# Performance work log

Measured on AMD Instinct MI355X. Metric: run time of the kernel, lower is better.

Reference implementation:

```python
import jax, jax.numpy as jnp
import numpy as np

T, B, D, H, O = 128, 256, 512, 1024, 20
THR = 1.0
ALPHA = float(np.exp(-1.0 / 20.0))  # exp(-dt/tau_m)
KAPPA = float(np.exp(-1.0 / 20.0))  # exp(-dt/tau_o)
B_O = 0.0


def setup_inputs() -> dict:
    key = jax.random.key(0)
    k1, k2, k3, k4 = jax.random.split(key, 4)
    x = jax.random.normal(k1, (T, B, D), dtype=jnp.float32)
    # kaiming_normal: std = sqrt(2/fan_in), gain = 1.0
    w_in = jax.random.normal(k2, (H, D), dtype=jnp.float32) * np.sqrt(2.0 / D)
    w_rec = jax.random.normal(k3, (H, H), dtype=jnp.float32) * np.sqrt(2.0 / H)
    w_out = jax.random.normal(k4, (O, H), dtype=jnp.float32) * np.sqrt(2.0 / H)
    return {"x": x, "w_in": w_in, "w_rec": w_rec, "w_out": w_out}


def reference(x, w_in, w_rec, w_out):
    # mask out self-recurrence (diagonal zeroed)
    w_rec_eff = w_rec * (1.0 - jnp.eye(w_rec.shape[0], dtype=w_rec.dtype))

    def step(carry, x_t):
        v, z, vo = carry
        v_new = ALPHA * v + z @ w_rec_eff.T + x_t @ w_in.T - z * THR
        z_new = (v_new > THR).astype(v_new.dtype)
        vo_new = KAPPA * vo + z_new @ w_out.T + B_O
        return (v_new, z_new, vo_new), vo_new

    v0 = jnp.zeros((x.shape[1], w_rec.shape[0]), dtype=x.dtype)
    vo0 = jnp.zeros((x.shape[1], w_out.shape[0]), dtype=x.dtype)
    # torch loop runs t = 0..T-2, consuming x[0..T-2]; vo[0] stays zero
    _, vo_rest = jax.lax.scan(step, (v0, v0, vo0), x[:-1])
    vo = jnp.concatenate([vo0[None], vo_rest], axis=0)  # [T, B, O]
    return jax.nn.softmax(vo, axis=2)
```

## Files before the change

kernel.cpp:

```cpp
#include <hip/hip_runtime.h>
#include <math.h>


#define T_ 128
#define B_ 256
#define D_ 512
#define H_ 1024
#define O_ 20
#define ST_ 127
#define WPB 32
#define ALPHA_F ((float)0.95122942450071400909)
#define KAPPA_F ((float)0.95122942450071400909)

typedef float v2f __attribute__((ext_vector_type(2)));

#if defined(__has_builtin)
#if __has_builtin(__builtin_elementwise_fma)
#define PK_FMA(a, b, c) __builtin_elementwise_fma(a, b, c)
#endif
#if __has_builtin(__builtin_amdgcn_global_load_lds)
#define HAVE_GLL 1
#endif
#endif
#ifndef PK_FMA
static __device__ inline v2f pk_fma_impl(v2f a, v2f b, v2f c) {
    v2f r; r[0] = __fmaf_rn(a[0], b[0], c[0]); r[1] = __fmaf_rn(a[1], b[1], c[1]);
    return r;
}
#define PK_FMA(a, b, c) pk_fma_impl(a, b, c)
#endif

static __device__ __forceinline__ void f2acc(float2& a, const float2 b) {
    a.x = __fadd_rn(a.x, b.x);
    a.y = __fadd_rn(a.y, b.y);
}

static __device__ __forceinline__ unsigned spread16(unsigned x) {
    x &= 0xFFFFu;
    x = (x | (x << 8)) & 0x00FF00FFu;
    x = (x | (x << 4)) & 0x0F0F0F0Fu;
    x = (x | (x << 2)) & 0x33333333u;
    x = (x | (x << 1)) & 0x55555555u;
    return x;
}

__global__ __launch_bounds__(256) void transpose_k(
    const float* __restrict__ src, float* __restrict__ dst,
    int rows, int cols, int zero_diag)
{
    __shared__ float tile[32][33];
    const int c0 = blockIdx.x * 32;
    const int r0 = blockIdx.y * 32;
    const int tid = threadIdx.x;
    const int lr = tid >> 3;
    const int lc = (tid & 7) * 4;
    const float4 vv = *(const float4*)(src + (size_t)(r0 + lr) * cols + c0 + lc);
    tile[lr][lc+0] = vv.x; tile[lr][lc+1] = vv.y;
    tile[lr][lc+2] = vv.z; tile[lr][lc+3] = vv.w;
    __syncthreads();
    const int wc = lr;
    const int wr = lc;
    float4 o;
    o.x = tile[wr+0][wc]; o.y = tile[wr+1][wc];
    o.z = tile[wr+2][wc]; o.w = tile[wr+3][wc];
    if (zero_diag) {
        const int c = c0 + wc;
        if (c == r0 + wr + 0) o.x = 0.f;
        if (c == r0 + wr + 1) o.y = 0.f;
        if (c == r0 + wr + 2) o.z = 0.f;
        if (c == r0 + wr + 3) o.w = 0.f;
    }
    *(float4*)(dst + (size_t)(c0 + wc) * rows + r0 + wr) = o;
}

__global__ __launch_bounds__(256) void srnn_init(
    float* __restrict__ v, unsigned* __restrict__ z0)
{
    const int i = blockIdx.x * 256 + threadIdx.x;
    if (i < B_ * H_)  v[i]  = 0.0f;
    if (i < B_ * WPB) z0[i] = 0u;
}

#define SWC(r) ((((r) >> 3) & 3) << 2)
__global__ __launch_bounds__(256) void srnn_qsum(
    const float* __restrict__ x,
    const float* __restrict__ WinT,
    float* __restrict__ qs,
    int s0, int nsl)
{
    __shared__ float wt[32][68];
    __shared__ float xt[32][68];
    const int nwg = nsl * 64;
    const int rb  = (int)blockIdx.x;
    const int lb  = (rb & 7) * (nwg >> 3) + (rb >> 3);
    const int sl = lb >> 6;
    const int t = lb & 63;
    const int h0 = (t & 15) << 6;
    const int b0 = (t >> 4) << 6;
    const int tid = threadIdx.x;
    const int tx4 = (tid & 15) << 2;
    const int ty4 = (tid >> 4) << 2;
    const float* xs = x + (size_t)(s0 + sl) * (B_ * D_);

    const int idxa = tid * 2, idxb = tid * 2 + 1;
    const int wra = idxa >> 4, wca = (idxa & 15) << 2;
    const int wrb = idxb >> 4, wcb = (idxb & 15) << 2;
    const int bra = idxa >> 3, kqa = (idxa & 7) << 2;
    const int brb = idxb >> 3, kqb = (idxb & 7) << 2;

    v2f accA[4][2], accB[4][2];
    #pragma unroll
    for (int i = 0; i < 4; ++i) {
        accA[i][0]=(v2f)0.f; accA[i][1]=(v2f)0.f;
        accB[i][0]=(v2f)0.f; accB[i][1]=(v2f)0.f;
    }

    float4 wp0, wp1, xp0, xp1;
    auto qload = [&](int kc) {
        wp0 = *(const float4*)(WinT + (size_t)(kc*32 + wra)*H_ + h0 + wca);
        wp1 = *(const float4*)(WinT + (size_t)(kc*32 + wrb)*H_ + h0 + wcb);
        xp0 = *(const float4*)(xs + (size_t)(b0+bra)*D_ + kc*32 + kqa);
        xp1 = *(const float4*)(xs + (size_t)(b0+brb)*D_ + kc*32 + kqb);
    };
    auto qstore = [&]() {
        *(float4*)&wt[wra][wca] = wp0;
        *(float4*)&wt[wrb][wcb] = wp1;
        xt[kqa+0][bra ^ SWC(kqa+0)]=xp0.x; xt[kqa+1][bra ^ SWC(kqa+1)]=xp0.y;
        xt[kqa+2][bra ^ SWC(kqa+2)]=xp0.z; xt[kqa+3][bra ^ SWC(kqa+3)]=xp0.w;
        xt[kqb+0][brb ^ SWC(kqb+0)]=xp1.x; xt[kqb+1][brb ^ SWC(kqb+1)]=xp1.y;
        xt[kqb+2][brb ^ SWC(kqb+2)]=xp1.z; xt[kqb+3][brb ^ SWC(kqb+3)]=xp1.w;
    };
    auto qinner = [&](v2f (&ACC)[4][2]) {
        #pragma unroll
        for (int kk = 0; kk < 32; ++kk) {
            const float4 zf = *(const float4*)&xt[kk][ty4 ^ SWC(kk)];
            const float4 wf = *(const float4*)&wt[kk][tx4];
            v2f wlo, whi;
            wlo[0]=wf.x; wlo[1]=wf.y; whi[0]=wf.z; whi[1]=wf.w;
            const float zz[4] = {zf.x, zf.y, zf.z, zf.w};
            #pragma unroll
            for (int i = 0; i < 4; ++i) {
                v2f zv; zv[0]=zz[i]; zv[1]=zz[i];
                ACC[i][0] = PK_FMA(zv, wlo, ACC[i][0]);
                ACC[i][1] = PK_FMA(zv, whi, ACC[i][1]);
            }
        }
    };

    qload(0);
    for (int kc = 0; kc < 10; ++kc) {
        __syncthreads();
        qstore();
        __syncthreads();
        qload(kc + 1);
        qinner(accA);
    }
    for (int kc = 10; kc < 16; ++kc) {
        __syncthreads();
        qstore();
        __syncthreads();
        if (kc < 15) qload(kc + 1);
        qinner(accB);
    }

    float* qd = qs + (size_t)sl * (B_ * H_);
    #pragma unroll
    for (int i = 0; i < 4; ++i) {
        float4 o;
        o.x = __fadd_rn(accA[i][0][0], accB[i][0][0]);
        o.y = __fadd_rn(accA[i][0][1], accB[i][0][1]);
        o.z = __fadd_rn(accA[i][1][0], accB[i][1][0]);
        o.w = __fadd_rn(accA[i][1][1], accB[i][1][1]);
        *(float4*)(qd + (size_t)(b0 + ty4 + i) * H_ + h0 + tx4) = o;
    }
}

#define STG_FLOATS (64 * 128)

static __device__ __forceinline__ void issue_stage(
    const float* __restrict__ WrecT, float (*wt)[STG_FLOATS],
    int s, int cb, int ht, int w, int ln)
{
#ifdef HAVE_GLL
    const int r2 = (ln >> 5);
    const int c4 = (ln & 31) << 2;
    #pragma unroll
    for (int i = 0; i < 4; ++i) {
        const int row = s * 64 + w * 8 + i * 2;
        const float* gs = WrecT + (size_t)(row + r2) * H_ + ht * 128 + c4;
        float* ld = &wt[cb][(w * 8 + i * 2) * 128];
        __builtin_amdgcn_global_load_lds(
            (const __attribute__((address_space(1))) void*)gs,
            (__attribute__((address_space(3))) void*)ld, 16, 0, 0);
    }
#else
    #pragma unroll
    for (int i = 0; i < 4; ++i) {
        const int row = s * 64 + w * 8 + i * 2 + (ln >> 5);
        const float4 tv = *(const float4*)(WrecT + (size_t)row * H_ + ht * 128 + ((ln & 31) << 2));
        *(float4*)&wt[cb][(w * 8 + i * 2) * 128 + ln * 4] = tv;
    }
#endif
}

#ifdef HAVE_GLL
#define WAITV4() asm volatile("s_waitcnt vmcnt(4)" ::: "memory")
#define WAITV0() asm volatile("s_waitcnt vmcnt(0)" ::: "memory")
#define STEPBAR() __builtin_amdgcn_s_barrier()
#else
#define WAITV4()
#define WAITV0()
#define STEPBAR() __syncthreads()
#endif

#define PROC_STAGE(ACC, SS, CB) do { \
    const int n_ = __builtin_amdgcn_readfirstlane(cntL[SS][w]); \
    const unsigned short* kl_ = klist2[SS][w]; \
    const char* wb_ = ((const char*)&wt[CB][0]) + (ln << 3); \
    int i_ = 0; \
    for (; i_ + 4 <= n_; i_ += 4) { \
        const uint2 kk_ = *(const uint2*)(kl_ + i_); \
        const float2 r0_ = *(const float2*)(wb_ + (kk_.x & 0xFFFFu)); \
        const float2 r1_ = *(const float2*)(wb_ + (kk_.x >> 16)); \
        const float2 r2_ = *(const float2*)(wb_ + (kk_.y & 0xFFFFu)); \
        const float2 r3_ = *(const float2*)(wb_ + (kk_.y >> 16)); \
        f2acc(ACC, r0_); f2acc(ACC, r1_); f2acc(ACC, r2_); f2acc(ACC, r3_); \
    } \
    if (i_ < n_) { \
        const uint2 kk_ = *(const uint2*)(kl_ + i_); \
        const float2 r0_ = *(const float2*)(wb_ + (kk_.x & 0xFFFFu)); \
        f2acc(ACC, r0_); \
        if (i_ + 1 < n_) { \
            const float2 r1_ = *(const float2*)(wb_ + (kk_.x >> 16)); \
            f2acc(ACC, r1_); \
        } \
        if (i_ + 2 < n_) { \
            const float2 r2_ = *(const float2*)(wb_ + (kk_.y & 0xFFFFu)); \
            f2acc(ACC, r2_); \
        } \
    } \
} while (0)

#define STEP_S(SS, ACC) do { \
    if ((SS) < 15) issue_stage(WrecT, wt, (SS) + 1, ((SS) + 1) & 1, ht, w, ln); \
    if ((SS) < 15) { WAITV4(); } else { WAITV0(); } \
    STEPBAR(); \
    asm volatile("" ::: "memory"); \
    PROC_STAGE(ACC, SS, (SS) & 1); \
    asm volatile("" ::: "memory"); \
    STEPBAR(); \
} while (0)

__global__ __launch_bounds__(512) void srnn_step(
    const float* __restrict__ WrecT,
    const float* __restrict__ qsum_s,
    const unsigned* __restrict__ zin,
    unsigned* __restrict__ zout,
    float* __restrict__ v)
{
    __shared__ float wt[2][STG_FLOATS];
    __shared__ unsigned short klist2[16][8][64];
    __shared__ int cntL[16][8];
    __shared__ unsigned zwsh[8][32];

    const int bid = (int)blockIdx.x;
    const int ht = bid & 7;
    const int bg = bid >> 3;
    const int tid = threadIdx.x;
    const int w = tid >> 6;
    const int ln = tid & 63;
    const int b = bg * 8 + w;

    unsigned zword = 0u;
    if (ln < 32) zword = zin[(size_t)b * WPB + ln];

    issue_stage(WrecT, wt, 0, 0, ht, w, ln);

    if (ln < 32) {
        zwsh[w][ln] = zword;
        const int myc = __popc(zword);
        const int ec = __shfl_up(myc, 1, 32);
        const int oc = __shfl_down(myc, 1, 32);
        if (!(ln & 1)) cntL[ln >> 1][w] = myc + oc;
        int ofs = (ln & 1) ? ec : 0;
        const unsigned kbase = (unsigned)((ln & 1) << 14);
        unsigned tw = zword;
        while (tw) {
            const int j = __builtin_ctz(tw);
            tw &= tw - 1;
            klist2[ln >> 1][w][ofs++] = (unsigned short)(kbase + ((unsigned)j << 9));
        }
    }

    float2 acc0 = {0.f, 0.f}, acc1 = {0.f, 0.f};
    float2 acc2 = {0.f, 0.f}, acc3 = {0.f, 0.f};

    STEP_S(0, acc0);  STEP_S(1, acc0);  STEP_S(2, acc0);  STEP_S(3, acc0);  STEP_S(4, acc0);
    STEP_S(5, acc1);  STEP_S(6, acc1);  STEP_S(7, acc1);  STEP_S(8, acc1);  STEP_S(9, acc1);
    STEP_S(10, acc2); STEP_S(11, acc2); STEP_S(12, acc2); STEP_S(13, acc2); STEP_S(14, acc2);
    STEP_S(15, acc3);

    const int h0 = ht * 128 + ln * 2;
    const size_t bh = (size_t)b * H_ + h0;
    const float2 qv = *(const float2*)(qsum_s + bh);
    const float2 vv = *(const float2*)(v + bh);
    const unsigned zwrd = zwsh[w][ht * 4 + (ln >> 4)];
    const int bb0 = (ln & 15) * 2;

    const float a0c[2] = {acc0.x, acc0.y};
    const float a1c[2] = {acc1.x, acc1.y};
    const float a2c[2] = {acc2.x, acc2.y};
    const float a3c[2] = {acc3.x, acc3.y};
    const float qc[2]  = {qv.x, qv.y};
    const float vc[2]  = {vv.x, vv.y};

    float vn2[2];
    #pragma unroll
    for (int m = 0; m < 2; ++m) {
        const float P  = __fadd_rn(__fadd_rn(__fadd_rn(a0c[m], a1c[m]), a2c[m]), a3c[m]);
        const float zs = ((zwrd >> (bb0 + m)) & 1u) ? 1.f : 0.f;
        const float t1 = __fmul_rn(ALPHA_F, vc[m]);
        const float t2 = __fadd_rn(t1, P);
        const float t3 = __fadd_rn(t2, qc[m]);
        vn2[m] = __fsub_rn(t3, zs);
    }
    float2 vst; vst.x = vn2[0]; vst.y = vn2[1];
    *(float2*)(v + bh) = vst;

    const unsigned long long bx = __ballot(vn2[0] > 1.0f);
    const unsigned long long by = __ballot(vn2[1] > 1.0f);
    if (ln < 4) {
        const unsigned ex = (unsigned)((bx >> (ln * 16)) & 0xFFFFull);
        const unsigned ey = (unsigned)((by >> (ln * 16)) & 0xFFFFull);
        const unsigned word = spread16(ex) | (spread16(ey) << 1);
        zout[(size_t)b * WPB + ht * 4 + ln] = word;
    }
}

__global__ __launch_bounds__(256) void srnn_zo(
    const unsigned* __restrict__ zhist,
    const float* __restrict__ w_out,
    float* __restrict__ zo)
{
    __shared__ float red[16][16][O_ + 1];
    const int s  = blockIdx.x >> 4;
    const int bg = blockIdx.x & 15;
    const int tid = threadIdx.x;
    const int bl  = tid >> 4;
    const int seg = tid & 15;
    const int b = bg * 16 + bl;
    const unsigned* zr = zhist + ((size_t)s * B_ + b) * WPB;
    const unsigned w0 = zr[seg * 2 + 0];
    const unsigned w1 = zr[seg * 2 + 1];

    float a[O_];
    #pragma unroll
    for (int o = 0; o < O_; ++o) a[o] = 0.f;
    const int hb = seg * 64;
    for (int j = 0; j < 32; ++j) {
        if ((w0 >> j) & 1u) {
            #pragma unroll
            for (int o = 0; o < O_; ++o) a[o] += w_out[(size_t)o * H_ + hb + j];
        }
    }
    for (int j = 0; j < 32; ++j) {
        if ((w1 >> j) & 1u) {
            #pragma unroll
            for (int o = 0; o < O_; ++o) a[o] += w_out[(size_t)o * H_ + hb + 32 + j];
        }
    }
    #pragma unroll
    for (int o = 0; o < O_; ++o) red[bl][seg][o] = a[o];
    __syncthreads();
    for (int ww = tid; ww < 16 * O_; ww += 256) {
        const int bl2 = ww / O_, o = ww % O_;
        float sum = 0.f;
        #pragma unroll
        for (int g = 0; g < 16; ++g) sum += red[bl2][g][o];
        zo[((size_t)s * B_ + bg * 16 + bl2) * O_ + o] = sum;
    }
}

__global__ __launch_bounds__(64) void srnn_scan(
    const float* __restrict__ zo,
    float* __restrict__ out)
{
    __shared__ float vos[T_][O_];
    const int b = blockIdx.x;
    const int tid = threadIdx.x;
    if (tid < O_) {
        float vo = 0.f;
        vos[0][tid] = 0.f;
        for (int sp = 0; sp < ST_; ++sp) {
            vo = KAPPA_F * vo + zo[((size_t)sp * B_ + b) * O_ + tid];
            vos[sp + 1][tid] = vo;
        }
    }
    __syncthreads();
    for (int t = tid; t < T_; t += 64) {
        float m = -1e30f;
        #pragma unroll
        for (int o = 0; o < O_; ++o) m = fmaxf(m, vos[t][o]);
        float e[O_];
        float ssum = 0.f;
        #pragma unroll
        for (int o = 0; o < O_; ++o) {
            const float ee = expf(vos[t][o] - m);
            e[o] = ee;
            ssum += ee;
        }
        const float inv = 1.f / ssum;
        #pragma unroll
        for (int o = 0; o < O_; ++o)
            out[((size_t)t * B_ + b) * O_ + o] = e[o] * inv;
    }
}

extern "C" void kernel_launch(void* const* d_in, const int* in_sizes, int n_in,
                              void* d_out, int out_size, void* d_ws, size_t ws_size,
                              hipStream_t stream) {
    const float* x     = (const float*)d_in[0];
    const float* w_in  = (const float*)d_in[1];
    const float* w_rec = (const float*)d_in[2];
    const float* w_out = (const float*)d_in[3];
    float* out = (float*)d_out;

    float*    WrecT = (float*)d_ws;
    float*    WinT  = WrecT + (size_t)H_ * H_;
    float*    v     = WinT  + (size_t)D_ * H_;
    unsigned* z0    = (unsigned*)(v + (size_t)B_ * H_);
    unsigned* zhist = z0 + (size_t)B_ * WPB;
    float*    zo    = (float*)(zhist + (size_t)ST_ * B_ * WPB);
    float*    qbuf  = zo + (size_t)ST_ * B_ * O_;

    const size_t used = (size_t)((char*)qbuf - (char*)d_ws);
    const size_t qstep = (size_t)B_ * H_ * sizeof(float);
    size_t avail = (ws_size > used) ? (ws_size - used) : 0;
    int G = (int)(avail / qstep);
    if (G < 1)  G = 1;
    if (G > ST_) G = ST_;

    transpose_k<<<dim3(32, 32), 256, 0, stream>>>(w_rec, WrecT, H_, H_, 1);
    transpose_k<<<dim3(16, 32), 256, 0, stream>>>(w_in,  WinT,  H_, D_, 0);
    srnn_init<<<(B_ * H_ + 255) / 256, 256, 0, stream>>>(v, z0);

    const unsigned* zprev = z0;
    for (int s0 = 0; s0 < ST_; s0 += G) {
        const int gc = (ST_ - s0 < G) ? (ST_ - s0) : G;
        srnn_qsum<<<gc * 64, 256, 0, stream>>>(x, WinT, qbuf, s0, gc);
        for (int sl = 0; sl < gc; ++sl) {
            const int s = s0 + sl;
            unsigned* zcur = zhist + (size_t)s * B_ * WPB;
            srnn_step<<<256, 512, 0, stream>>>(
                WrecT, qbuf + (size_t)sl * B_ * H_, zprev, zcur, v);
            zprev = zcur;
        }
    }

    srnn_zo<<<ST_ * 16, 256, 0, stream>>>(zhist, w_out, zo);
    srnn_scan<<<B_, 64, 0, stream>>>(zo, out);
}
```

Baseline: 2.811 ms.

## Triple-buffer W_rec stages with one barrier per step and register-held spike lists

The recurrent step kernel now streams W_rec in 32-row stages through a three-slot LDS ring. Each stage is prefetched two steps ahead and only one barrier runs per stage instead of two. The per-word spike counts and words now come from wave shuffles rather than shared-memory tables, and the sparse-gather inner loop is unrolled by eight. This is meant to reduce barrier stalls and overlap global-to-LDS copies with the gather work. In exchange the kernel runs twice as many stages, and summation order changes, which could flip spike thresholds.

```diff
diff --git a/kernel.cpp b/kernel.cpp
--- a/kernel.cpp
+++ b/kernel.cpp
@@ -175,80 +175,82 @@
     }
 }
 
-#define STG_FLOATS (64 * 128)
+#define STG_FLOATS (32 * 128)
 
 static __device__ __forceinline__ void issue_stage(
     const float* __restrict__ WrecT, float (*wt)[STG_FLOATS],
-    int s, int cb, int ht, int w, int ln)
+    int s, int cb, int ht, int w, int tid)
 {
 #ifdef HAVE_GLL
-    const int r2 = (ln >> 5);
-    const int c4 = (ln & 31) << 2;
-    #pragma unroll
-    for (int i = 0; i < 4; ++i) {
-        const int row = s * 64 + w * 8 + i * 2;
-        const float* gs = WrecT + (size_t)(row + r2) * H_ + ht * 128 + c4;
-        float* ld = &wt[cb][(w * 8 + i * 2) * 128];
+    #pragma unroll
+    for (int i = 0; i < 2; ++i) {
+        const int row = s * 32 + i * 16 + (tid >> 5);
+        const float* gs = WrecT + (size_t)row * H_ + ht * 128 + ((tid & 31) << 2);
+        float* ld = &wt[cb][i * 2048 + w * 256];
         __builtin_amdgcn_global_load_lds(
             (const __attribute__((address_space(1))) void*)gs,
             (__attribute__((address_space(3))) void*)ld, 16, 0, 0);
     }
 #else
     #pragma unroll
-    for (int i = 0; i < 4; ++i) {
-        const int row = s * 64 + w * 8 + i * 2 + (ln >> 5);
-        const float4 tv = *(const float4*)(WrecT + (size_t)row * H_ + ht * 128 + ((ln & 31) << 2));
-        *(float4*)&wt[cb][(w * 8 + i * 2) * 128 + ln * 4] = tv;
+    for (int i = 0; i < 2; ++i) {
+        const int row = s * 32 + i * 16 + (tid >> 5);
+        const float4 tv = *(const float4*)(WrecT + (size_t)row * H_ + ht * 128 + ((tid & 31) << 2));
+        *(float4*)&wt[cb][i * 2048 + tid * 4] = tv;
     }
 #endif
 }
 
 #ifdef HAVE_GLL
-#define WAITV4() asm volatile("s_waitcnt vmcnt(4)" ::: "memory")
+#define WAITV2() asm volatile("s_waitcnt vmcnt(2)" ::: "memory")
 #define WAITV0() asm volatile("s_waitcnt vmcnt(0)" ::: "memory")
 #define STEPBAR() __builtin_amdgcn_s_barrier()
 #else
-#define WAITV4()
+#define WAITV2()
 #define WAITV0()
 #define STEPBAR() __syncthreads()
 #endif
 
-#define PROC_STAGE(ACC, SS, CB) do { \
-    const int n_ = __builtin_amdgcn_readfirstlane(cntL[SS][w]); \
-    const unsigned short* kl_ = klist2[SS][w]; \
-    const char* wb_ = ((const char*)&wt[CB][0]) + (ln << 3); \
+#define PROC_STAGE(SS, ACC) do { \
+    const int n_ = __builtin_amdgcn_readfirstlane(__shfl((int)myc, (SS), 64)); \
+    const unsigned short* kl_ = &klist2[SS][w][0]; \
+    const char* wb_ = ((const char*)&wt[(SS) % 3][0]) + (ln << 3); \
     int i_ = 0; \
-    for (; i_ + 4 <= n_; i_ += 4) { \
+    for (; i_ + 8 <= n_; i_ += 8) { \
+        const uint4 kk_ = *(const uint4*)(kl_ + i_); \
+        const float2 r0_ = *(const float2*)(wb_ + (kk_.x & 0xFFFFu)); \
+        const float2 r1_ = *(const float2*)(wb_ + (kk_.x >> 16)); \
+        const float2 r2_ = *(const float2*)(wb_ + (kk_.y & 0xFFFFu)); \
+        const float2 r3_ = *(const float2*)(wb_ + (kk_.y >> 16)); \
+        const float2 r4_ = *(const float2*)(wb_ + (kk_.z & 0xFFFFu)); \
+        const float2 r5_ = *(const float2*)(wb_ + (kk_.z >> 16)); \
+        const float2 r6_ = *(const float2*)(wb_ + (kk_.w & 0xFFFFu)); \
+        const float2 r7_ = *(const float2*)(wb_ + (kk_.w >> 16)); \
+        f2acc(ACC, r0_); f2acc(ACC, r1_); f2acc(ACC, r2_); f2acc(ACC, r3_); \
+        f2acc(ACC, r4_); f2acc(ACC, r5_); f2acc(ACC, r6_); f2acc(ACC, r7_); \
+    } \
+    if (i_ + 4 <= n_) { \
         const uint2 kk_ = *(const uint2*)(kl_ + i_); \
         const float2 r0_ = *(const float2*)(wb_ + (kk_.x & 0xFFFFu)); \
         const float2 r1_ = *(const float2*)(wb_ + (kk_.x >> 16)); \
         const float2 r2_ = *(const float2*)(wb_ + (kk_.y & 0xFFFFu)); \
         const float2 r3_ = *(const float2*)(wb_ + (kk_.y >> 16)); \
         f2acc(ACC, r0_); f2acc(ACC, r1_); f2acc(ACC, r2_); f2acc(ACC, r3_); \
+        i_ += 4; \
     } \
-    if (i_ < n_) { \
-        const uint2 kk_ = *(const uint2*)(kl_ + i_); \
-        const float2 r0_ = *(const float2*)(wb_ + (kk_.x & 0xFFFFu)); \
-        f2acc(ACC, r0_); \
-        if (i_ + 1 < n_) { \
-            const float2 r1_ = *(const float2*)(wb_ + (kk_.x >> 16)); \
-            f2acc(ACC, r1_); \
-        } \
-        if (i_ + 2 < n_) { \
-            const float2 r2_ = *(const float2*)(wb_ + (kk_.y & 0xFFFFu)); \
-            f2acc(ACC, r2_); \
-        } \
+    for (; i_ < n_; ++i_) { \
+        const float2 r_ = *(const float2*)(wb_ + kl_[i_]); \
+        f2acc(ACC, r_); \
     } \
 } while (0)
 
 #define STEP_S(SS, ACC) do { \
-    if ((SS) < 15) issue_stage(WrecT, wt, (SS) + 1, ((SS) + 1) & 1, ht, w, ln); \
-    if ((SS) < 15) { WAITV4(); } else { WAITV0(); } \
+    if ((SS) < 31) { WAITV2(); } else { WAITV0(); } \
     STEPBAR(); \
     asm volatile("" ::: "memory"); \
-    PROC_STAGE(ACC, SS, (SS) & 1); \
+    if ((SS) < 30) issue_stage(WrecT, wt, (SS) + 2, ((SS) + 2) % 3, ht, w, tid); \
+    PROC_STAGE(SS, ACC); \
     asm volatile("" ::: "memory"); \
-    STEPBAR(); \
 } while (0)
 
 __global__ __launch_bounds__(512) void srnn_step(
@@ -258,10 +260,8 @@
     unsigned* __restrict__ zout,
     float* __restrict__ v)
 {
-    __shared__ float wt[2][STG_FLOATS];
-    __shared__ unsigned short klist2[16][8][64];
-    __shared__ int cntL[16][8];
-    __shared__ unsigned zwsh[8][32];
+    __shared__ float wt[3][STG_FLOATS];
+    __shared__ unsigned short klist2[32][8][32];
 
     const int bid = (int)blockIdx.x;
     const int ht = bid & 7;
@@ -274,21 +274,18 @@
     unsigned zword = 0u;
     if (ln < 32) zword = zin[(size_t)b * WPB + ln];
 
-    issue_stage(WrecT, wt, 0, 0, ht, w, ln);
-
+    issue_stage(WrecT, wt, 0, 0, ht, w, tid);
+    issue_stage(WrecT, wt, 1, 1, ht, w, tid);
+
+    const int myc = __popc(zword);
     if (ln < 32) {
-        zwsh[w][ln] = zword;
-        const int myc = __popc(zword);
-        const int ec = __shfl_up(myc, 1, 32);
-        const int oc = __shfl_down(myc, 1, 32);
-        if (!(ln & 1)) cntL[ln >> 1][w] = myc + oc;
-        int ofs = (ln & 1) ? ec : 0;
-        const unsigned kbase = (unsigned)((ln & 1) << 14);
+        unsigned short* kd = &klist2[ln][w][0];
+        int ofs = 0;
         unsigned tw = zword;
         while (tw) {
             const int j = __builtin_ctz(tw);
             tw &= tw - 1;
-            klist2[ln >> 1][w][ofs++] = (unsigned short)(kbase + ((unsigned)j << 9));
+            kd[ofs++] = (unsigned short)((unsigned)j << 9);
         }
     }
 
@@ -296,15 +293,18 @@
     float2 acc2 = {0.f, 0.f}, acc3 = {0.f, 0.f};
 
     STEP_S(0, acc0);  STEP_S(1, acc0);  STEP_S(2, acc0);  STEP_S(3, acc0);  STEP_S(4, acc0);
-    STEP_S(5, acc1);  STEP_S(6, acc1);  STEP_S(7, acc1);  STEP_S(8, acc1);  STEP_S(9, acc1);
-    STEP_S(10, acc2); STEP_S(11, acc2); STEP_S(12, acc2); STEP_S(13, acc2); STEP_S(14, acc2);
-    STEP_S(15, acc3);
+    STEP_S(5, acc0);  STEP_S(6, acc0);  STEP_S(7, acc0);  STEP_S(8, acc0);  STEP_S(9, acc0);
+    STEP_S(10, acc1); STEP_S(11, acc1); STEP_S(12, acc1); STEP_S(13, acc1); STEP_S(14, acc1);
+    STEP_S(15, acc1); STEP_S(16, acc1); STEP_S(17, acc1); STEP_S(18, acc1); STEP_S(19, acc1);
+    STEP_S(20, acc2); STEP_S(21, acc2); STEP_S(22, acc2); STEP_S(23, acc2); STEP_S(24, acc2);
+    STEP_S(25, acc2); STEP_S(26, acc2); STEP_S(27, acc2); STEP_S(28, acc2); STEP_S(29, acc2);
+    STEP_S(30, acc3); STEP_S(31, acc3);
 
     const int h0 = ht * 128 + ln * 2;
     const size_t bh = (size_t)b * H_ + h0;
     const float2 qv = *(const float2*)(qsum_s + bh);
     const float2 vv = *(const float2*)(v + bh);
-    const unsigned zwrd = zwsh[w][ht * 4 + (ln >> 4)];
+    const unsigned zwrd = (unsigned)__shfl((int)zword, ht * 4 + (ln >> 4), 64);
     const int bb0 = (ln & 15) * 2;
 
     const float a0c[2] = {acc0.x, acc0.y};
```

Result: slower. 3.038 ms (+8.1%).
